# Kernel optimization log

Measured on AMD Instinct MI355X. Metric: run time of the kernel, lower is better.

The kernel has to match this reference:

```python
import jax, jax.numpy as jnp
import numpy as np


def setup_inputs() -> dict:
    key = jax.random.key(0)
    ks = jax.random.split(key, 6)
    N, T, D, H = 256, 128, 512, 512
    x = jax.random.normal(ks[0], (N, T, D), dtype=jnp.float32)
    A = jax.random.normal(ks[1], (N, H, 4, 4), dtype=jnp.float32)
    Wx = jax.random.normal(ks[2], (D, 4 * H), dtype=jnp.float32) / np.sqrt(D)
    Wh = jax.random.normal(ks[3], (H, 4 * H), dtype=jnp.float32) / np.sqrt(H)
    Wattn = jax.random.normal(ks[4], (H, 4 * H), dtype=jnp.float32) / np.sqrt(H)
    b = jnp.zeros((4 * H,), dtype=jnp.float32)
    return {"x": x, "A": A, "Wx": Wx, "Wh": Wh, "Wattn": Wattn, "b": b}


def reference(x, A, Wx, Wh, Wattn, b):
    N, T, D = x.shape
    H = Wh.shape[0]
    A_flat = A.reshape(N, H, -1)  # (N, H, 16)
    h0 = A_flat.mean(axis=-1)     # mean over 4x4 grid
    c0 = h0
    inv_sqrt_H = 1.0 / np.sqrt(H).astype(np.float32)

    def step(carry, x_t):
        h, c = carry
        # scaled dot-product attention over the 16 spatial cells
        scores = jnp.einsum('nh,nhp->np', h, A_flat) * inv_sqrt_H  # (N, 16)
        w = jax.nn.softmax(scores, axis=-1)
        attn = jnp.einsum('nhp,np->nh', A_flat, w)                 # (N, H)
        a = x_t @ Wx + h @ Wh + attn @ Wattn + b                   # (N, 4H)
        a_i, a_f, a_o, a_g = jnp.split(a, 4, axis=1)
        i = jax.nn.sigmoid(a_i)
        f = jax.nn.sigmoid(a_f)
        o = jax.nn.sigmoid(a_o)
        g = jnp.tanh(a_g)
        c_next = f * c + i * g
        h_next = o * jnp.tanh(c_next)
        return (h_next, c_next), h_next

    _, hs = jax.lax.scan(step, (h0, c0), jnp.swapaxes(x, 0, 1))  # (T, N, H)
    return jnp.swapaxes(hs, 0, 1)  # (N, T, H)
```

## Files before the change

kernel.cpp:

```cpp
#include <hip/hip_runtime.h>
#include <math.h>

typedef unsigned short u16;
typedef _Float16 h16;
typedef _Float16 f16x8 __attribute__((ext_vector_type(8)));
typedef float f32x4 __attribute__((ext_vector_type(4)));

__device__ __forceinline__ float sigm(float x) { return 1.f / (1.f + expf(-x)); }


__global__ void k_pack_w(const float* __restrict__ Wx, const float* __restrict__ Wh,
                         h16* __restrict__ WhiS, h16* __restrict__ WloS) {
  unsigned idx = blockIdx.x * 256 + threadIdx.x;
  unsigned e = idx & 7, l = (idx >> 3) & 63, cf = (idx >> 9) & 1;
  unsigned t2 = idx >> 10;
  unsigned j = t2 >> 5, ks = t2 & 31;
  unsigned k = ks * 32 + ((l >> 4) << 3) + e;
  unsigned c32 = cf * 16 + (l & 15);
  unsigned acol = (c32 >> 3) * 512 + j * 8 + (c32 & 7);
  float v = (k < 512) ? Wx[(size_t)k * 2048 + acol]
                      : Wh[(size_t)(k - 512) * 2048 + acol];
  h16 hi = (h16)v;
  WhiS[idx] = hi;
  WloS[idx] = (h16)((v - (float)hi) * 4096.f);
}

__global__ void k_af_pack(const float* __restrict__ Af, h16* __restrict__ afhi,
                          h16* __restrict__ aflo) {
  unsigned idx = blockIdx.x * 256 + threadIdx.x;
  unsigned e = idx & 7, l = (idx >> 3) & 63, ksg = (idx >> 9) & 15, n = idx >> 13;
  unsigned k = ksg * 32 + ((l >> 4) << 3) + e;
  float v = Af[(size_t)n * 8192 + k * 16 + (l & 15)];
  h16 hi = (h16)v;
  afhi[idx] = hi;
  aflo[idx] = (h16)((v - (float)hi) * 4096.f);
}

__global__ void k_wat_pack(const float* __restrict__ Wat, h16* __restrict__ wathi,
                           h16* __restrict__ watlo) {
  unsigned idx = blockIdx.x * 256 + threadIdx.x;
  unsigned e = idx & 7, l = (idx >> 3) & 63, ksg = (idx >> 9) & 15, cg = idx >> 13;
  unsigned k = ksg * 32 + ((l >> 4) << 3) + e;
  float v = Wat[(size_t)k * 2048 + cg * 16 + (l & 15)];
  h16 hi = (h16)v;
  wathi[idx] = hi;
  watlo[idx] = (h16)((v - (float)hi) * 4096.f);
}

__global__ __launch_bounds__(256) void k_m(const h16* __restrict__ afhi,
                                           const h16* __restrict__ aflo,
                                           const h16* __restrict__ wathi,
                                           const h16* __restrict__ watlo,
                                           float* __restrict__ M2) {
  const int tid = threadIdx.x;
  const int ct = blockIdx.x, ng = blockIdx.y;
  const int l = tid & 63, w = tid >> 6;
  const int cg = ct * 4 + w;
  const int col = cg * 16 + (l & 15);
  const int lq = l >> 4;
  f32x4 acc1[8], acc2[8];
#pragma unroll
  for (int i = 0; i < 8; ++i) {
    acc1[i] = (f32x4){0.f, 0.f, 0.f, 0.f};
    acc2[i] = (f32x4){0.f, 0.f, 0.f, 0.f};
  }
  for (int ksg = 0; ksg < 16; ++ksg) {
    const size_t boff = (((size_t)cg * 16 + ksg) * 64 + l) * 8;
    const f16x8 bh = *(const f16x8*)(wathi + boff);
    const f16x8 bl = *(const f16x8*)(watlo + boff);
#pragma unroll
    for (int i = 0; i < 8; ++i) {
      const size_t aoff = (((size_t)(ng * 8 + i) * 16 + ksg) * 64 + l) * 8;
      const f16x8 ah = *(const f16x8*)(afhi + aoff);
      const f16x8 al = *(const f16x8*)(aflo + aoff);
      acc1[i] = __builtin_amdgcn_mfma_f32_16x16x32_f16(ah, bh, acc1[i], 0, 0, 0);
      acc2[i] = __builtin_amdgcn_mfma_f32_16x16x32_f16(al, bh, acc2[i], 0, 0, 0);
      acc2[i] = __builtin_amdgcn_mfma_f32_16x16x32_f16(ah, bl, acc2[i], 0, 0, 0);
    }
  }
#pragma unroll
  for (int i = 0; i < 8; ++i) {
    float4 o;
    o.x = acc1[i][0] + acc2[i][0] * (1.f / 4096.f);
    o.y = acc1[i][1] + acc2[i][1] * (1.f / 4096.f);
    o.z = acc1[i][2] + acc2[i][2] * (1.f / 4096.f);
    o.w = acc1[i][3] + acc2[i][3] * (1.f / 4096.f);
    *(float4*)(M2 + ((size_t)(ng * 8 + i) * 2048 + col) * 16 + lq * 4) = o;
  }
}

__global__ void k_xsplit(const float* __restrict__ x, h16* __restrict__ xfhi,
                         h16* __restrict__ xflo) {
  unsigned tg = blockIdx.x * 256 + threadIdx.x;
  unsigned l = tg & 63, rt = (tg >> 6) & 1, ksg = (tg >> 7) & 15;
  unsigned g = (tg >> 11) & 7, t = tg >> 14;
  int n = g * 32 + rt * 16 + (l & 15);
  int k0 = ksg * 32 + (l >> 4) * 8;
  const float* xp = x + ((size_t)n * 128 + t) * 512 + k0;
  f32x4 v0 = *(const f32x4*)xp, v1 = *(const f32x4*)(xp + 4);
  float vv[8] = {v0[0], v0[1], v0[2], v0[3], v1[0], v1[1], v1[2], v1[3]};
  union { h16 h[8]; uint4 u; } a, b;
#pragma unroll
  for (int e = 0; e < 8; ++e) {
    h16 hh = (h16)vv[e];
    a.h[e] = hh;
    b.h[e] = (h16)((vv[e] - (float)hh) * 4096.f);
  }
  *(uint4*)(xfhi + (size_t)tg * 8) = a.u;
  *(uint4*)(xflo + (size_t)tg * 8) = b.u;
}

__global__ __launch_bounds__(512) void k_init(const float* __restrict__ Af,
                                              h16* __restrict__ hfhi,
                                              h16* __restrict__ hflo,
                                              float* __restrict__ cst,
                                              float* __restrict__ sb0) {
  const int n = blockIdx.x, k = threadIdx.x;
  float Areg[16];
  const f32x4* A4 = (const f32x4*)(Af + (size_t)n * 8192 + k * 16);
#pragma unroll
  for (int q4 = 0; q4 < 4; ++q4) {
    f32x4 v = A4[q4];
#pragma unroll
    for (int e = 0; e < 4; ++e) Areg[q4 * 4 + e] = v[e];
  }
  float s = 0.f;
#pragma unroll
  for (int p = 0; p < 16; ++p) s += Areg[p];
  s *= 0.0625f;
  cst[n * 512 + k] = s;
  h16 hh = (h16)s;
  const int g = n >> 5;
  const int hoff = ((((g * 16 + (k >> 5)) * 2 + ((n >> 4) & 1)) * 64 +
                     ((n & 15) | (((k >> 3) & 3) << 4))) * 8) + (k & 7);
  hfhi[hoff] = hh;
  hflo[hoff] = (h16)((s - (float)hh) * 4096.f);
  float ps[16];
#pragma unroll
  for (int p = 0; p < 16; ++p) ps[p] = s * Areg[p];
#pragma unroll
  for (int m = 1; m <= 4; m <<= 1)
#pragma unroll
    for (int p = 0; p < 16; ++p) ps[p] += __shfl_xor(ps[p], m);
  if ((k & 7) == 0) {
    float* o = sb0 + ((size_t)n * 64 + (k >> 3)) * 16;
#pragma unroll
    for (int p = 0; p < 16; ++p) o[p] = ps[p];
  }
}

template<bool XPRE>
__global__ __launch_bounds__(512, 4) void k_step(
    const float* __restrict__ bv, const float* __restrict__ Af,
    const float* __restrict__ x, const h16* __restrict__ xfhi, const h16* __restrict__ xflo,
    const h16* __restrict__ WhiS, const h16* __restrict__ WloS,
    const float* __restrict__ Mws,
    const float* __restrict__ sbR, float* __restrict__ sbW,
    h16* __restrict__ hfhi, h16* __restrict__ hflo,
    float* __restrict__ cst, float* __restrict__ out, int t) {
  __shared__ float P[7 * 1056];
  __shared__ float wsh[32][17];

  const int tid = threadIdx.x;
  const int l = tid & 63, wv = tid >> 6;
  const int bid = blockIdx.x;
  const int g = bid >> 6;
  const int j = (bid & 7) * 8 + ((bid >> 3) & 7);
  const int n0 = g * 32;

  {
    const int nS = tid >> 4, pS = tid & 15;
    const float* sr = sbR + ((size_t)(n0 + nS) * 64) * 16 + pS;
    float s = 0.f;
#pragma unroll 8
    for (int jj = 0; jj < 64; ++jj) s += sr[jj * 16];
    s *= 0.04419417382415922f;
    float m = s;
#pragma unroll
    for (int o = 8; o >= 1; o >>= 1) m = fmaxf(m, __shfl_xor(m, o, 16));
    float e = __expf(s - m);
    float se = e;
#pragma unroll
    for (int o = 8; o >= 1; o >>= 1) se += __shfl_xor(se, o, 16);
    wsh[nS][pS] = e / se;
  }

  const h16* whiJ = WhiS + (size_t)j * 32768;
  const h16* wloJ = WloS + (size_t)j * 32768;

  const int rC = tid >> 3, qC = tid & 7;
  const int colC = j * 8 + qC;
  const float b_i = bv[colC], b_f = bv[512 + colC], b_o = bv[1024 + colC],
              b_g = bv[1536 + colC];

  const int rb = t & 1, wb = rb ^ 1;
  const h16* hfhiR = hfhi + (size_t)rb * 131072;
  const h16* hfloR = hflo + (size_t)rb * 131072;

  f32x4 acc1[2][2], acc2[2][2];
#pragma unroll
  for (int rt = 0; rt < 2; ++rt)
#pragma unroll
    for (int cf = 0; cf < 2; ++cf) {
      acc1[rt][cf] = (f32x4){0.f, 0.f, 0.f, 0.f};
      acc2[rt][cf] = (f32x4){0.f, 0.f, 0.f, 0.f};
    }

  auto kstep = [&](int ksg) {
    const f16x8 bh0 = *(const f16x8*)(whiJ + ((size_t)(ksg * 2 + 0) * 64 + l) * 8);
    const f16x8 bh1 = *(const f16x8*)(whiJ + ((size_t)(ksg * 2 + 1) * 64 + l) * 8);
    const f16x8 bl0 = *(const f16x8*)(wloJ + ((size_t)(ksg * 2 + 0) * 64 + l) * 8);
    const f16x8 bl1 = *(const f16x8*)(wloJ + ((size_t)(ksg * 2 + 1) * 64 + l) * 8);
    f16x8 Ah[2], Al[2];
    if (ksg < 16) {
      if (XPRE) {
#pragma unroll
        for (int rt = 0; rt < 2; ++rt) {
          const size_t base = ((((size_t)t * 8 + g) * 16 + ksg) * 2 + rt) * 512 + l * 8;
          Ah[rt] = *(const f16x8*)(xfhi + base);
          Al[rt] = *(const f16x8*)(xflo + base);
        }
      } else {
#pragma unroll
        for (int rt = 0; rt < 2; ++rt) {
          const int n_x = g * 32 + rt * 16 + (l & 15);
          const int k_x = ksg * 32 + (l >> 4) * 8;
          const float* xp = x + ((size_t)n_x * 128 + t) * 512 + k_x;
          f32x4 v0 = *(const f32x4*)xp, v1 = *(const f32x4*)(xp + 4);
          float vv[8] = {v0[0], v0[1], v0[2], v0[3], v1[0], v1[1], v1[2], v1[3]};
#pragma unroll
          for (int e = 0; e < 8; ++e) {
            h16 hh = (h16)vv[e];
            Ah[rt][e] = hh;
            Al[rt][e] = (h16)((vv[e] - (float)hh) * 4096.f);
          }
        }
      }
    } else {
#pragma unroll
      for (int rt = 0; rt < 2; ++rt) {
        const size_t base = (((size_t)(g * 16 + (ksg - 16)) * 2 + rt) * 64 + l) * 8;
        Ah[rt] = *(const f16x8*)(hfhiR + base);
        Al[rt] = *(const f16x8*)(hfloR + base);
      }
    }
#pragma unroll
    for (int rt = 0; rt < 2; ++rt) {
      acc1[rt][0] = __builtin_amdgcn_mfma_f32_16x16x32_f16(Ah[rt], bh0, acc1[rt][0], 0, 0, 0);
      acc1[rt][1] = __builtin_amdgcn_mfma_f32_16x16x32_f16(Ah[rt], bh1, acc1[rt][1], 0, 0, 0);
      acc2[rt][0] = __builtin_amdgcn_mfma_f32_16x16x32_f16(Al[rt], bh0, acc2[rt][0], 0, 0, 0);
      acc2[rt][1] = __builtin_amdgcn_mfma_f32_16x16x32_f16(Al[rt], bh1, acc2[rt][1], 0, 0, 0);
      acc2[rt][0] = __builtin_amdgcn_mfma_f32_16x16x32_f16(Ah[rt], bl0, acc2[rt][0], 0, 0, 0);
      acc2[rt][1] = __builtin_amdgcn_mfma_f32_16x16x32_f16(Ah[rt], bl1, acc2[rt][1], 0, 0, 0);
    }
  };

#pragma unroll
  for (int i = 0; i < 4; ++i) kstep(wv + 8 * i);

  float accf[2][2][4];
#pragma unroll
  for (int rt = 0; rt < 2; ++rt)
#pragma unroll
    for (int cf = 0; cf < 2; ++cf)
#pragma unroll
      for (int rg = 0; rg < 4; ++rg)
        accf[rt][cf][rg] = acc1[rt][cf][rg] + acc2[rt][cf][rg] * (1.f / 4096.f);

  auto publish = [&](int slot) {
#pragma unroll
    for (int rt = 0; rt < 2; ++rt)
#pragma unroll
      for (int cf = 0; cf < 2; ++cf)
#pragma unroll
        for (int rg = 0; rg < 4; ++rg)
          P[slot * 1056 + (rt * 16 + (l >> 4) * 4 + rg) * 33 + cf * 16 + (l & 15)] =
              accf[rt][cf][rg];
  };
  auto addin = [&](int slot) {
#pragma unroll
    for (int rt = 0; rt < 2; ++rt)
#pragma unroll
      for (int cf = 0; cf < 2; ++cf)
#pragma unroll
        for (int rg = 0; rg < 4; ++rg)
          accf[rt][cf][rg] +=
              P[slot * 1056 + (rt * 16 + (l >> 4) * 4 + rg) * 33 + cf * 16 + (l & 15)];
  };

  if (wv >= 4) publish(wv - 4);
  __syncthreads();
  if (wv < 4) addin(wv);
  if (wv == 2) publish(4);
  if (wv == 3) publish(5);
  __syncthreads();
  if (wv == 0) addin(4);
  if (wv == 1) { addin(5); publish(6); }
  __syncthreads();
  if (wv == 0) { addin(6); publish(0); }
  __syncthreads();

  if (tid < 256) {
    const float* Mr = Mws + ((size_t)(n0 + rC) * 2048 + colC) * 16;
    float am[4];
#pragma unroll
    for (int f = 0; f < 4; ++f) {
      const float* mp = Mr + (size_t)f * 8192;
      float s = 0.f;
#pragma unroll
      for (int p = 0; p < 16; ++p) s += wsh[rC][p] * mp[p];
      am[f] = s;
    }
    float ai = P[rC * 33 + qC] + am[0] + b_i;
    float af_ = P[rC * 33 + 8 + qC] + am[1] + b_f;
    float ao = P[rC * 33 + 16 + qC] + am[2] + b_o;
    float ag = P[rC * 33 + 24 + qC] + am[3] + b_g;
    float ig = sigm(ai), fg = sigm(af_), og = sigm(ao), gg = tanhf(ag);
    const size_t cix = (size_t)(n0 + rC) * 512 + colC;
    float c = cst[cix];
    float cn = fg * c + ig * gg;
    cst[cix] = cn;
    float hn = og * tanhf(cn);
    h16 hh = (h16)hn;
    const int hoff = ((((g * 16 + (j >> 2)) * 2 + (rC >> 4)) * 64 +
                       ((rC & 15) | ((j & 3) << 4))) * 8) + qC;
    hfhi[(size_t)wb * 131072 + hoff] = hh;
    hflo[(size_t)wb * 131072 + hoff] = (h16)((hn - (float)hh) * 4096.f);
    out[((size_t)(n0 + rC) * 128 + t) * 512 + colC] = hn;

    float Areg[16];
    const f32x4* A4 = (const f32x4*)(Af + ((size_t)(n0 + rC) * 512 + colC) * 16);
#pragma unroll
    for (int q4 = 0; q4 < 4; ++q4) {
      f32x4 v = A4[q4];
#pragma unroll
      for (int e = 0; e < 4; ++e) Areg[q4 * 4 + e] = v[e];
    }
    float ps[16];
#pragma unroll
    for (int p = 0; p < 16; ++p) ps[p] = hn * Areg[p];
#pragma unroll
    for (int m = 1; m <= 4; m <<= 1)
#pragma unroll
      for (int p = 0; p < 16; ++p) ps[p] += __shfl_xor(ps[p], m);
    if (qC == 0) {
      float* o = sbW + ((size_t)(n0 + rC) * 64 + j) * 16;
#pragma unroll
      for (int p = 0; p < 16; ++p) o[p] = ps[p];
    }
  }
}


extern "C" void kernel_launch(void* const* d_in, const int* in_sizes, int n_in,
                              void* d_out, int out_size, void* d_ws, size_t ws_size,
                              hipStream_t stream) {
  (void)in_sizes; (void)n_in; (void)out_size;
  const float* x   = (const float*)d_in[0];
  const float* Af  = (const float*)d_in[1];
  const float* Wx  = (const float*)d_in[2];
  const float* Wh  = (const float*)d_in[3];
  const float* Wat = (const float*)d_in[4];
  const float* bv  = (const float*)d_in[5];
  float* out = (float*)d_out;

  char* ws = (char*)d_ws;
  size_t off = 0;
  auto alloc = [&](size_t nb) {
    char* p = ws + off; off = (off + nb + 255) & ~(size_t)255; return p;
  };
  h16*   WhiS = (h16*)alloc(2097152ull * 2);
  h16*   WloS = (h16*)alloc(2097152ull * 2);
  float* Mws  = (float*)alloc(8388608ull * 4);
  float* sb   = (float*)alloc(2ull * 262144 * 4);
  h16*   hfhi = (h16*)alloc(262144ull * 2);
  h16*   hflo = (h16*)alloc(262144ull * 2);
  float* cst  = (float*)alloc(131072ull * 4);
  size_t base_end = off;
  h16* xfhi = (h16*)alloc(16777216ull * 2);
  h16* xflo = (h16*)alloc(16777216ull * 2);
  bool xpre = (ws_size >= base_end + 2ull * 16777216ull * 2 + 4096);

  h16* afhi  = xfhi;
  h16* aflo  = xfhi + 2097152;
  h16* wathi = xfhi + 2ull * 2097152;
  h16* watlo = xfhi + 3ull * 2097152;

  k_pack_w<<<8192, 256, 0, stream>>>(Wx, Wh, WhiS, WloS);
  k_af_pack<<<8192, 256, 0, stream>>>(Af, afhi, aflo);
  k_wat_pack<<<4096, 256, 0, stream>>>(Wat, wathi, watlo);
  k_m<<<dim3(32, 32), 256, 0, stream>>>(afhi, aflo, wathi, watlo, Mws);
  k_init<<<256, 512, 0, stream>>>(Af, hfhi, hflo, cst, sb);
  if (xpre) k_xsplit<<<8192, 256, 0, stream>>>(x, xfhi, xflo);

  for (int t = 0; t < 128; ++t) {
    const float* sbR = sb + (size_t)(t & 1) * 262144;
    float* sbW = (float*)sb + (size_t)((t + 1) & 1) * 262144;
    if (xpre)
      k_step<true><<<512, 512, 0, stream>>>(bv, Af, x, xfhi, xflo, WhiS, WloS, Mws,
                                            sbR, sbW, hfhi, hflo, cst, out, t);
    else
      k_step<false><<<512, 512, 0, stream>>>(bv, Af, x, xfhi, xflo, WhiS, WloS, Mws,
                                             sbR, sbW, hfhi, hflo, cst, out, t);
  }
}
```

Measured before the change: 2.269 ms.

## Interleave hi/lo fp16 split buffers and flatten the cross-wave reduction

Stores the hi and lo fp16 halves of the weights, x and h next to each other per lane (32 contiguous bytes) instead of in separate arrays, so each lane fetches both halves from one region. The step kernel's three-round tree reduction across 8 waves, with three barriers, becomes one publish of all 8 partials to shared memory, a single barrier, and a serial 8-way sum in the gate threads. The M precompute also splits its correction accumulator in two to shorten MFMA dependency chains. Shared memory grows by one slot, and the gate threads now do more LDS reads.

```diff
diff --git a/kernel.cpp b/kernel.cpp
--- a/kernel.cpp
+++ b/kernel.cpp
@@ -10,10 +10,10 @@
 
 
 __global__ void k_pack_w(const float* __restrict__ Wx, const float* __restrict__ Wh,
-                         h16* __restrict__ WhiS, h16* __restrict__ WloS) {
+                         h16* __restrict__ WS) {
   unsigned idx = blockIdx.x * 256 + threadIdx.x;
-  unsigned e = idx & 7, l = (idx >> 3) & 63, cf = (idx >> 9) & 1;
-  unsigned t2 = idx >> 10;
+  unsigned e = idx & 7, hl = (idx >> 3) & 1, l = (idx >> 4) & 63, cf = (idx >> 10) & 1;
+  unsigned t2 = idx >> 11;
   unsigned j = t2 >> 5, ks = t2 & 31;
   unsigned k = ks * 32 + ((l >> 4) << 3) + e;
   unsigned c32 = cf * 16 + (l & 15);
@@ -21,8 +21,7 @@
   float v = (k < 512) ? Wx[(size_t)k * 2048 + acol]
                       : Wh[(size_t)(k - 512) * 2048 + acol];
   h16 hi = (h16)v;
-  WhiS[idx] = hi;
-  WloS[idx] = (h16)((v - (float)hi) * 4096.f);
+  WS[idx] = hl ? (h16)((v - (float)hi) * 4096.f) : hi;
 }
 
 __global__ void k_af_pack(const float* __restrict__ Af, h16* __restrict__ afhi,
@@ -58,11 +57,12 @@
   const int cg = ct * 4 + w;
   const int col = cg * 16 + (l & 15);
   const int lq = l >> 4;
-  f32x4 acc1[8], acc2[8];
+  f32x4 acc1[8], acc2a[8], acc2b[8];
 #pragma unroll
   for (int i = 0; i < 8; ++i) {
     acc1[i] = (f32x4){0.f, 0.f, 0.f, 0.f};
-    acc2[i] = (f32x4){0.f, 0.f, 0.f, 0.f};
+    acc2a[i] = (f32x4){0.f, 0.f, 0.f, 0.f};
+    acc2b[i] = (f32x4){0.f, 0.f, 0.f, 0.f};
   }
   for (int ksg = 0; ksg < 16; ++ksg) {
     const size_t boff = (((size_t)cg * 16 + ksg) * 64 + l) * 8;
@@ -73,24 +73,23 @@
       const size_t aoff = (((size_t)(ng * 8 + i) * 16 + ksg) * 64 + l) * 8;
       const f16x8 ah = *(const f16x8*)(afhi + aoff);
       const f16x8 al = *(const f16x8*)(aflo + aoff);
-      acc1[i] = __builtin_amdgcn_mfma_f32_16x16x32_f16(ah, bh, acc1[i], 0, 0, 0);
-      acc2[i] = __builtin_amdgcn_mfma_f32_16x16x32_f16(al, bh, acc2[i], 0, 0, 0);
-      acc2[i] = __builtin_amdgcn_mfma_f32_16x16x32_f16(ah, bl, acc2[i], 0, 0, 0);
+      acc1[i]  = __builtin_amdgcn_mfma_f32_16x16x32_f16(ah, bh, acc1[i], 0, 0, 0);
+      acc2a[i] = __builtin_amdgcn_mfma_f32_16x16x32_f16(al, bh, acc2a[i], 0, 0, 0);
+      acc2b[i] = __builtin_amdgcn_mfma_f32_16x16x32_f16(ah, bl, acc2b[i], 0, 0, 0);
     }
   }
 #pragma unroll
   for (int i = 0; i < 8; ++i) {
     float4 o;
-    o.x = acc1[i][0] + acc2[i][0] * (1.f / 4096.f);
-    o.y = acc1[i][1] + acc2[i][1] * (1.f / 4096.f);
-    o.z = acc1[i][2] + acc2[i][2] * (1.f / 4096.f);
-    o.w = acc1[i][3] + acc2[i][3] * (1.f / 4096.f);
+    o.x = acc1[i][0] + (acc2a[i][0] + acc2b[i][0]) * (1.f / 4096.f);
+    o.y = acc1[i][1] + (acc2a[i][1] + acc2b[i][1]) * (1.f / 4096.f);
+    o.z = acc1[i][2] + (acc2a[i][2] + acc2b[i][2]) * (1.f / 4096.f);
+    o.w = acc1[i][3] + (acc2a[i][3] + acc2b[i][3]) * (1.f / 4096.f);
     *(float4*)(M2 + ((size_t)(ng * 8 + i) * 2048 + col) * 16 + lq * 4) = o;
   }
 }
 
-__global__ void k_xsplit(const float* __restrict__ x, h16* __restrict__ xfhi,
-                         h16* __restrict__ xflo) {
+__global__ void k_xsplit(const float* __restrict__ x, h16* __restrict__ xf) {
   unsigned tg = blockIdx.x * 256 + threadIdx.x;
   unsigned l = tg & 63, rt = (tg >> 6) & 1, ksg = (tg >> 7) & 15;
   unsigned g = (tg >> 11) & 7, t = tg >> 14;
@@ -106,13 +105,12 @@
     a.h[e] = hh;
     b.h[e] = (h16)((vv[e] - (float)hh) * 4096.f);
   }
-  *(uint4*)(xfhi + (size_t)tg * 8) = a.u;
-  *(uint4*)(xflo + (size_t)tg * 8) = b.u;
+  *(uint4*)(xf + (size_t)tg * 16) = a.u;
+  *(uint4*)(xf + (size_t)tg * 16 + 8) = b.u;
 }
 
 __global__ __launch_bounds__(512) void k_init(const float* __restrict__ Af,
-                                              h16* __restrict__ hfhi,
-                                              h16* __restrict__ hflo,
+                                              h16* __restrict__ hf,
                                               float* __restrict__ cst,
                                               float* __restrict__ sb0) {
   const int n = blockIdx.x, k = threadIdx.x;
@@ -131,10 +129,10 @@
   cst[n * 512 + k] = s;
   h16 hh = (h16)s;
   const int g = n >> 5;
-  const int hoff = ((((g * 16 + (k >> 5)) * 2 + ((n >> 4) & 1)) * 64 +
-                     ((n & 15) | (((k >> 3) & 3) << 4))) * 8) + (k & 7);
-  hfhi[hoff] = hh;
-  hflo[hoff] = (h16)((s - (float)hh) * 4096.f);
+  const int hbase = ((((g * 16 + (k >> 5)) * 2 + ((n >> 4) & 1)) * 64 +
+                      ((n & 15) | (((k >> 3) & 3) << 4))) * 2) * 8;
+  hf[hbase + (k & 7)] = hh;
+  hf[hbase + 8 + (k & 7)] = (h16)((s - (float)hh) * 4096.f);
   float ps[16];
 #pragma unroll
   for (int p = 0; p < 16; ++p) ps[p] = s * Areg[p];
@@ -152,13 +150,11 @@
 template<bool XPRE>
 __global__ __launch_bounds__(512, 4) void k_step(
     const float* __restrict__ bv, const float* __restrict__ Af,
-    const float* __restrict__ x, const h16* __restrict__ xfhi, const h16* __restrict__ xflo,
-    const h16* __restrict__ WhiS, const h16* __restrict__ WloS,
-    const float* __restrict__ Mws,
+    const float* __restrict__ x, const h16* __restrict__ xf,
+    const h16* __restrict__ WS, const float* __restrict__ Mws,
     const float* __restrict__ sbR, float* __restrict__ sbW,
-    h16* __restrict__ hfhi, h16* __restrict__ hflo,
-    float* __restrict__ cst, float* __restrict__ out, int t) {
-  __shared__ float P[7 * 1056];
+    h16* __restrict__ hf, float* __restrict__ cst, float* __restrict__ out, int t) {
+  __shared__ float P[8 * 1056];
   __shared__ float wsh[32][17];
 
   const int tid = threadIdx.x;
@@ -185,8 +181,7 @@
     wsh[nS][pS] = e / se;
   }
 
-  const h16* whiJ = WhiS + (size_t)j * 32768;
-  const h16* wloJ = WloS + (size_t)j * 32768;
+  const h16* wJ = WS + (size_t)j * 65536;
 
   const int rC = tid >> 3, qC = tid & 7;
   const int colC = j * 8 + qC;
@@ -194,8 +189,7 @@
               b_g = bv[1536 + colC];
 
   const int rb = t & 1, wb = rb ^ 1;
-  const h16* hfhiR = hfhi + (size_t)rb * 131072;
-  const h16* hfloR = hflo + (size_t)rb * 131072;
+  const h16* hfR = hf + (size_t)rb * 262144;
 
   f32x4 acc1[2][2], acc2[2][2];
 #pragma unroll
@@ -207,18 +201,20 @@
     }
 
   auto kstep = [&](int ksg) {
-    const f16x8 bh0 = *(const f16x8*)(whiJ + ((size_t)(ksg * 2 + 0) * 64 + l) * 8);
-    const f16x8 bh1 = *(const f16x8*)(whiJ + ((size_t)(ksg * 2 + 1) * 64 + l) * 8);
-    const f16x8 bl0 = *(const f16x8*)(wloJ + ((size_t)(ksg * 2 + 0) * 64 + l) * 8);
-    const f16x8 bl1 = *(const f16x8*)(wloJ + ((size_t)(ksg * 2 + 1) * 64 + l) * 8);
+    const size_t w0 = (((size_t)ksg * 2 + 0) * 64 + l) * 16;
+    const size_t w1 = (((size_t)ksg * 2 + 1) * 64 + l) * 16;
+    const f16x8 bh0 = *(const f16x8*)(wJ + w0);
+    const f16x8 bl0 = *(const f16x8*)(wJ + w0 + 8);
+    const f16x8 bh1 = *(const f16x8*)(wJ + w1);
+    const f16x8 bl1 = *(const f16x8*)(wJ + w1 + 8);
     f16x8 Ah[2], Al[2];
     if (ksg < 16) {
       if (XPRE) {
 #pragma unroll
         for (int rt = 0; rt < 2; ++rt) {
-          const size_t base = ((((size_t)t * 8 + g) * 16 + ksg) * 2 + rt) * 512 + l * 8;
-          Ah[rt] = *(const f16x8*)(xfhi + base);
-          Al[rt] = *(const f16x8*)(xflo + base);
+          const size_t base = (((((size_t)t * 8 + g) * 16 + ksg) * 2 + rt) * 64 + l) * 16;
+          Ah[rt] = *(const f16x8*)(xf + base);
+          Al[rt] = *(const f16x8*)(xf + base + 8);
         }
       } else {
 #pragma unroll
@@ -239,9 +235,9 @@
     } else {
 #pragma unroll
       for (int rt = 0; rt < 2; ++rt) {
-        const size_t base = (((size_t)(g * 16 + (ksg - 16)) * 2 + rt) * 64 + l) * 8;
-        Ah[rt] = *(const f16x8*)(hfhiR + base);
-        Al[rt] = *(const f16x8*)(hfloR + base);
+        const size_t base = ((((size_t)(g * 16 + (ksg - 16)) * 2 + rt) * 64 + l)) * 16;
+        Ah[rt] = *(const f16x8*)(hfR + base);
+        Al[rt] = *(const f16x8*)(hfR + base + 8);
       }
     }
 #pragma unroll
@@ -258,63 +254,39 @@
 #pragma unroll
   for (int i = 0; i < 4; ++i) kstep(wv + 8 * i);
 
-  float accf[2][2][4];
 #pragma unroll
   for (int rt = 0; rt < 2; ++rt)
 #pragma unroll
     for (int cf = 0; cf < 2; ++cf)
 #pragma unroll
       for (int rg = 0; rg < 4; ++rg)
-        accf[rt][cf][rg] = acc1[rt][cf][rg] + acc2[rt][cf][rg] * (1.f / 4096.f);
-
-  auto publish = [&](int slot) {
-#pragma unroll
-    for (int rt = 0; rt < 2; ++rt)
-#pragma unroll
-      for (int cf = 0; cf < 2; ++cf)
-#pragma unroll
-        for (int rg = 0; rg < 4; ++rg)
-          P[slot * 1056 + (rt * 16 + (l >> 4) * 4 + rg) * 33 + cf * 16 + (l & 15)] =
-              accf[rt][cf][rg];
-  };
-  auto addin = [&](int slot) {
-#pragma unroll
-    for (int rt = 0; rt < 2; ++rt)
-#pragma unroll
-      for (int cf = 0; cf < 2; ++cf)
-#pragma unroll
-        for (int rg = 0; rg < 4; ++rg)
-          accf[rt][cf][rg] +=
-              P[slot * 1056 + (rt * 16 + (l >> 4) * 4 + rg) * 33 + cf * 16 + (l & 15)];
-  };
-
-  if (wv >= 4) publish(wv - 4);
-  __syncthreads();
-  if (wv < 4) addin(wv);
-  if (wv == 2) publish(4);
-  if (wv == 3) publish(5);
-  __syncthreads();
-  if (wv == 0) addin(4);
-  if (wv == 1) { addin(5); publish(6); }
-  __syncthreads();
-  if (wv == 0) { addin(6); publish(0); }
+        P[wv * 1056 + (rt * 16 + (l >> 4) * 4 + rg) * 33 + cf * 16 + (l & 15)] =
+            acc1[rt][cf][rg] + acc2[rt][cf][rg] * (1.f / 4096.f);
   __syncthreads();
 
   if (tid < 256) {
     const float* Mr = Mws + ((size_t)(n0 + rC) * 2048 + colC) * 16;
-    float am[4];
+    float av[4];
 #pragma unroll
     for (int f = 0; f < 4; ++f) {
       const float* mp = Mr + (size_t)f * 8192;
       float s = 0.f;
 #pragma unroll
       for (int p = 0; p < 16; ++p) s += wsh[rC][p] * mp[p];
-      am[f] = s;
-    }
-    float ai = P[rC * 33 + qC] + am[0] + b_i;
-    float af_ = P[rC * 33 + 8 + qC] + am[1] + b_f;
-    float ao = P[rC * 33 + 16 + qC] + am[2] + b_o;
-    float ag = P[rC * 33 + 24 + qC] + am[3] + b_g;
+      av[f] = s;
+    }
+#pragma unroll
+    for (int f = 0; f < 4; ++f) {
+      const int pidx = rC * 33 + f * 8 + qC;
+      float s = av[f];
+#pragma unroll
+      for (int sl = 0; sl < 8; ++sl) s += P[sl * 1056 + pidx];
+      av[f] = s;
+    }
+    float ai = av[0] + b_i;
+    float af_ = av[1] + b_f;
+    float ao = av[2] + b_o;
+    float ag = av[3] + b_g;
     float ig = sigm(ai), fg = sigm(af_), og = sigm(ao), gg = tanhf(ag);
     const size_t cix = (size_t)(n0 + rC) * 512 + colC;
     float c = cst[cix];
@@ -322,10 +294,10 @@
     cst[cix] = cn;
     float hn = og * tanhf(cn);
     h16 hh = (h16)hn;
-    const int hoff = ((((g * 16 + (j >> 2)) * 2 + (rC >> 4)) * 64 +
-                       ((rC & 15) | ((j & 3) << 4))) * 8) + qC;
-    hfhi[(size_t)wb * 131072 + hoff] = hh;
-    hflo[(size_t)wb * 131072 + hoff] = (h16)((hn - (float)hh) * 4096.f);
+    const int hbase = ((((g * 16 + (j >> 2)) * 2 + (rC >> 4)) * 64 +
+                        ((rC & 15) | ((j & 3) << 4))) * 2) * 8;
+    hf[(size_t)wb * 262144 + hbase + qC] = hh;
+    hf[(size_t)wb * 262144 + hbase + 8 + qC] = (h16)((hn - (float)hh) * 4096.f);
     out[((size_t)(n0 + rC) * 128 + t) * 512 + colC] = hn;
 
     float Areg[16];
@@ -369,38 +341,35 @@
   auto alloc = [&](size_t nb) {
     char* p = ws + off; off = (off + nb + 255) & ~(size_t)255; return p;
   };
-  h16*   WhiS = (h16*)alloc(2097152ull * 2);
-  h16*   WloS = (h16*)alloc(2097152ull * 2);
+  h16*   WS   = (h16*)alloc(4194304ull * 2);
   float* Mws  = (float*)alloc(8388608ull * 4);
   float* sb   = (float*)alloc(2ull * 262144 * 4);
-  h16*   hfhi = (h16*)alloc(262144ull * 2);
-  h16*   hflo = (h16*)alloc(262144ull * 2);
+  h16*   hf   = (h16*)alloc(524288ull * 2);
   float* cst  = (float*)alloc(131072ull * 4);
   size_t base_end = off;
-  h16* xfhi = (h16*)alloc(16777216ull * 2);
-  h16* xflo = (h16*)alloc(16777216ull * 2);
-  bool xpre = (ws_size >= base_end + 2ull * 16777216ull * 2 + 4096);
-
-  h16* afhi  = xfhi;
-  h16* aflo  = xfhi + 2097152;
-  h16* wathi = xfhi + 2ull * 2097152;
-  h16* watlo = xfhi + 3ull * 2097152;
-
-  k_pack_w<<<8192, 256, 0, stream>>>(Wx, Wh, WhiS, WloS);
+  h16* xf = (h16*)alloc(33554432ull * 2);
+  bool xpre = (ws_size >= base_end + 33554432ull * 2 + 4096);
+
+  h16* afhi  = xf;
+  h16* aflo  = xf + 2097152;
+  h16* wathi = xf + 2ull * 2097152;
+  h16* watlo = xf + 3ull * 2097152;
+
+  k_pack_w<<<16384, 256, 0, stream>>>(Wx, Wh, WS);
   k_af_pack<<<8192, 256, 0, stream>>>(Af, afhi, aflo);
   k_wat_pack<<<4096, 256, 0, stream>>>(Wat, wathi, watlo);
   k_m<<<dim3(32, 32), 256, 0, stream>>>(afhi, aflo, wathi, watlo, Mws);
-  k_init<<<256, 512, 0, stream>>>(Af, hfhi, hflo, cst, sb);
-  if (xpre) k_xsplit<<<8192, 256, 0, stream>>>(x, xfhi, xflo);
+  k_init<<<256, 512, 0, stream>>>(Af, hf, cst, sb);
+  if (xpre) k_xsplit<<<8192, 256, 0, stream>>>(x, xf);
 
   for (int t = 0; t < 128; ++t) {
     const float* sbR = sb + (size_t)(t & 1) * 262144;
     float* sbW = (float*)sb + (size_t)((t + 1) & 1) * 262144;
     if (xpre)
-      k_step<true><<<512, 512, 0, stream>>>(bv, Af, x, xfhi, xflo, WhiS, WloS, Mws,
-                                            sbR, sbW, hfhi, hflo, cst, out, t);
+      k_step<true><<<512, 512, 0, stream>>>(bv, Af, x, xf, WS, Mws,
+                                            sbR, sbW, hf, cst, out, t);
     else
-      k_step<false><<<512, 512, 0, stream>>>(bv, Af, x, xfhi, xflo, WhiS, WloS, Mws,
-                                             sbR, sbW, hfhi, hflo, cst, out, t);
-  }
-}
+      k_step<false><<<512, 512, 0, stream>>>(bv, Af, x, xf, WS, Mws,
+                                             sbR, sbW, hf, cst, out, t);
+  }
+}
```

Measured after the change: 2.293 ms. About the same (+1.1%).
